# Kernel optimization log

Hardware: AMD Instinct MI355X
Metric: run time of the kernel (lower is better)

The kernel has to match this reference:

```python
import jax, jax.numpy as jnp
import numpy as np

N, T, V = 64, 512, 25
L = 2 * V
M = N * T * V          # total graph nodes after flattening
E = 2_000_000          # number of directed edges
DIM_NODE, HIDDEN = 2, 20
BN_EPS = 1e-5


def setup_inputs() -> dict:
    key = jax.random.key(0)
    ks = jax.random.split(key, 8)
    x = jax.random.normal(ks[0], (N, T, L), dtype=jnp.float32)
    edge_index = jax.random.randint(ks[1], (2, E), 0, M, dtype=jnp.int64)
    # GCNConv(2 -> 20): weight + bias (PyG applies lin before propagate, bias after)
    W1 = jax.random.normal(ks[2], (DIM_NODE, HIDDEN), dtype=jnp.float32) * (1.0 / np.sqrt(DIM_NODE))
    b1 = jnp.zeros((HIDDEN,), dtype=jnp.float32)
    # BatchNorm1d(20) affine params
    gamma = jnp.ones((HIDDEN,), dtype=jnp.float32)
    beta = jnp.zeros((HIDDEN,), dtype=jnp.float32)
    # GCNConv(20 -> 2)
    W2 = jax.random.normal(ks[3], (HIDDEN, DIM_NODE), dtype=jnp.float32) * (1.0 / np.sqrt(HIDDEN))
    b2 = jnp.zeros((DIM_NODE,), dtype=jnp.float32)
    return {"x": x, "edge_index": edge_index, "W1": W1, "b1": b1,
            "gamma": gamma, "beta": beta, "W2": W2, "b2": b2}


def _gcn_conv(h, row, col, norm, W, b, num_nodes):
    # PyG GCNConv: linear transform, normalized gather-scatter aggregation, bias.
    h = h @ W                                            # [M, d_out]
    msg = h[row] * norm[:, None]                         # gather + scale  [E+M, d_out]
    out = jax.ops.segment_sum(msg, col, num_segments=num_nodes)
    return out + b


def reference(x, edge_index, W1, b1, gamma, beta, W2, b2):
    n, t, l = x.shape
    v = l // 2
    m = n * t * v
    xf = x.reshape(m, 2)

    # gcn_norm with add_self_loops=True, symmetric normalization
    self_loop = jnp.arange(m, dtype=edge_index.dtype)
    row = jnp.concatenate([edge_index[0], self_loop])
    col = jnp.concatenate([edge_index[1], self_loop])
    deg = jax.ops.segment_sum(jnp.ones(row.shape[0], dtype=x.dtype), col, num_segments=m)
    dinv = jnp.where(deg > 0, jax.lax.rsqrt(deg), 0.0)
    norm = dinv[row] * dinv[col]

    h = _gcn_conv(xf, row, col, norm, W1, b1, m)         # [M, 20]

    # BatchNorm1d in training mode: biased batch statistics over node dim
    mean = jnp.mean(h, axis=0)
    var = jnp.mean(jnp.square(h - mean), axis=0)
    h = (h - mean) * jax.lax.rsqrt(var + BN_EPS) * gamma + beta
    h = jax.nn.relu(h)

    out = _gcn_conv(h, row, col, norm, W2, b2, m)        # [M, 2]
    return out.reshape(n, t, l)
```

## Files before the change

kernel.cpp:

```cpp
#include <hip/hip_runtime.h>
#include <stdint.h>

#define MNODES (64*512*25)
#define NEDGES 2000000
#define HID 20
#define BN_EPSF 1e-5f

#define NB 800
#define BSHIFT 10
#define BNODES 1024
#define CAP 3072
#define RB 1024
#define EPT 16
#define CHUNK (RB*EPT)
#define SB 512

typedef unsigned long long ull;

#define QSCALE 2048.0f
#define INV_Q  (1.0f/2048.0f)
#define FBIAS 65536

__device__ inline unsigned int pack_src(float x, float y){
    int ix = __float2int_rn(fminf(fmaxf(x, -15.9f), 15.9f) * QSCALE);
    int iy = __float2int_rn(fminf(fmaxf(y, -15.9f), 15.9f) * QSCALE);
    return ((unsigned int)(unsigned short)(short)ix) |
           (((unsigned int)(unsigned short)(short)iy) << 16);
}
__device__ inline ull msg_to_add(unsigned int m){
    int sx = (int)(short)(m & 0xffffu);
    int sy = (int)(short)(m >> 16);
    return ((ull)(unsigned int)(sx + FBIAS) << 38) | (1ull << 26)
         | (ull)(unsigned int)(sy + FBIAS);
}
__device__ inline void unpack_acc(ull a, int& ix, int& iy, int& cnt){
    cnt = (int)((a >> 26) & 0xFFFu);
    iy  = (int)(a & 0x3FFFFFFu) - cnt * FBIAS;
    ix  = (int)(a >> 38)        - cnt * FBIAS;
}


__global__ __launch_bounds__(RB) void k_reorder(const void* ei,
                                                unsigned int* binned,
                                                unsigned int* counts){
    __shared__ unsigned int lhist[NB];
    __shared__ unsigned int lbase[NB];
    __shared__ unsigned int sflag;
    int tid = threadIdx.x;
    if (tid == 0) sflag = 0;
    for (int i = tid; i < NB; i += RB) lhist[i] = 0;
    __syncthreads();
    if (tid < 128){
        unsigned int a = ((const unsigned int*)ei)[2*tid + 1];
        if (a) atomicOr(&sflag, 1u);
    }
    __syncthreads();
    bool is32 = (sflag != 0);

    unsigned int ent[EPT];
    int bkt[EPT];
    bool ok[EPT];
    #pragma unroll
    for (int k = 0; k < EPT; ++k){
        int e = blockIdx.x*CHUNK + k*RB + tid;
        ok[k] = (e < NEDGES);
        if (ok[k]){
            unsigned int r, c;
            if (is32){
                const int* p = (const int*)ei;
                r = (unsigned int)p[e]; c = (unsigned int)p[NEDGES + e];
            } else {
                const long long* p = (const long long*)ei;
                r = (unsigned int)p[e]; c = (unsigned int)p[NEDGES + e];
            }
            bkt[k] = (int)(c >> BSHIFT);
            ent[k] = r | ((c & (BNODES-1)) << 20);
            atomicAdd(&lhist[bkt[k]], 1u);
        }
    }
    __syncthreads();
    for (int i = tid; i < NB; i += RB){
        lbase[i] = (unsigned int)(i*CAP) + atomicAdd(&counts[i], lhist[i]);
        lhist[i] = 0;
    }
    __syncthreads();
    #pragma unroll
    for (int k = 0; k < EPT; ++k){
        if (ok[k]){
            int b = bkt[k];
            unsigned int pos = lbase[b] + atomicAdd(&lhist[b], 1u);
            if (pos < (unsigned int)((b+1)*CAP)) binned[pos] = ent[k];
        }
    }
}


template<bool FINAL>
__global__ __launch_bounds__(SB) void k_scatter_bin(const unsigned int* __restrict__ binned,
                                                    const unsigned int* __restrict__ counts,
                                                    const unsigned int* __restrict__ srcq,
                                                    float* outbuf,
                                                    unsigned short* deg16,
                                                    const float* __restrict__ b2,
                                                    float* stats){
    __shared__ ull accs[BNODES];
    __shared__ float ss[8];
    int b = blockIdx.x, tid = threadIdx.x;
    int base = b*BNODES;
    if (!FINAL && tid < 8) ss[tid] = 0.0f;
    #pragma unroll
    for (int n = tid; n < BNODES; n += SB)
        accs[n] = msg_to_add(srcq[base + n]);
    __syncthreads();

    unsigned int start = (unsigned int)(b*CAP);
    unsigned int cnt_b = counts[b];
    unsigned int end   = start + (cnt_b < CAP ? cnt_b : CAP);
    unsigned int i = start + tid;
    for (; i + 3u*SB < end; i += 4u*SB){
        unsigned int m0 = binned[i];
        unsigned int m1 = binned[i +   SB];
        unsigned int m2 = binned[i + 2u*SB];
        unsigned int m3 = binned[i + 3u*SB];
        unsigned int s0 = srcq[m0 & 0xfffffu];
        unsigned int s1 = srcq[m1 & 0xfffffu];
        unsigned int s2v = srcq[m2 & 0xfffffu];
        unsigned int s3 = srcq[m3 & 0xfffffu];
        atomicAdd(&accs[m0 >> 20], msg_to_add(s0));
        atomicAdd(&accs[m1 >> 20], msg_to_add(s1));
        atomicAdd(&accs[m2 >> 20], msg_to_add(s2v));
        atomicAdd(&accs[m3 >> 20], msg_to_add(s3));
    }
    for (; i < end; i += SB){
        unsigned int m = binned[i];
        atomicAdd(&accs[m >> 20], msg_to_add(srcq[m & 0xfffffu]));
    }
    __syncthreads();

    float su=0.f, sv=0.f, suu=0.f, suv=0.f, svv=0.f;
    #pragma unroll
    for (int n = tid; n < BNODES; n += SB){
        int ix, iy, dg;
        unpack_acc(accs[n], ix, iy, dg);
        float d = rsqrtf((float)dg);
        float u = (float)ix * INV_Q * d;
        float v = (float)iy * INV_Q * d;
        if (FINAL){
            float2 o; o.x = u + b2[0]; o.y = v + b2[1];
            ((float2*)outbuf)[base + n] = o;
        } else {
            deg16[base + n] = (unsigned short)dg;
            float2 o; o.x = u; o.y = v;
            ((float2*)outbuf)[base + n] = o;
            su += u; sv += v; suu += u*u; suv += u*v; svv += v*v;
        }
    }
    if (!FINAL){
        #pragma unroll
        for (int off=32; off; off>>=1){
            su  += __shfl_down(su,  off, 64);
            sv  += __shfl_down(sv,  off, 64);
            suu += __shfl_down(suu, off, 64);
            suv += __shfl_down(suv, off, 64);
            svv += __shfl_down(svv, off, 64);
        }
        if ((tid & 63) == 0){
            atomicAdd(&ss[0], su);  atomicAdd(&ss[1], sv);
            atomicAdd(&ss[2], suu); atomicAdd(&ss[3], suv);
            atomicAdd(&ss[4], svv);
        }
        __syncthreads();
        if (tid < 5) atomicAdd(&stats[tid], ss[tid]);
    }
}

__global__ __launch_bounds__(SB) void k_prepq(const unsigned int* __restrict__ binned,
                                              const unsigned int* __restrict__ counts,
                                              const float* __restrict__ xf,
                                              unsigned int* xnq){
    __shared__ unsigned int cnt[BNODES];
    int b = blockIdx.x, tid = threadIdx.x;
    #pragma unroll
    for (int n = tid; n < BNODES; n += SB) cnt[n] = 0;
    __syncthreads();
    unsigned int start = (unsigned int)(b*CAP);
    unsigned int cnt_b = counts[b];
    unsigned int end   = start + (cnt_b < CAP ? cnt_b : CAP);
    for (unsigned int i = start + tid; i < end; i += SB)
        atomicAdd(&cnt[binned[i] >> 20], 1u);
    __syncthreads();
    int base = b*BNODES;
    #pragma unroll
    for (int n = tid; n < BNODES; n += SB){
        float d = rsqrtf((float)(cnt[n] + 1u));
        float2 xv = ((const float2*)xf)[base + n];
        xnq[base + n] = pack_src(xv.x*d, xv.y*d);
    }
}

__global__ void k_project(const float* __restrict__ s2,
                          const unsigned short* __restrict__ deg16,
                          const float* __restrict__ W1, const float* __restrict__ b1,
                          const float* __restrict__ stats,
                          const float* __restrict__ gamma, const float* __restrict__ beta,
                          const float* __restrict__ W2,
                          unsigned int* pq){
    __shared__ float sc[2*HID];
    int tid = threadIdx.x;
    if (tid < HID){
        const float invM = 1.0f / (float)MNODES;
        float Su  = stats[0]*invM, Sv  = stats[1]*invM;
        float Suu = stats[2]*invM, Suv = stats[3]*invM, Svv = stats[4]*invM;
        float a = W1[tid], bb = W1[HID+tid], c = b1[tid];
        float mean = a*Su + bb*Sv + c;
        float ex2  = a*a*Suu + 2.f*a*bb*Suv + bb*bb*Svv
                   + 2.f*a*c*Su + 2.f*bb*c*Sv + c*c;
        float var  = ex2 - mean*mean;
        float inv  = rsqrtf(var + BN_EPSF);
        float scale = gamma[tid]*inv;
        sc[tid]     = scale;
        sc[HID+tid] = beta[tid] - mean*scale;
    }
    __syncthreads();
    int i = blockIdx.x*blockDim.x + tid;
    if (i >= MNODES) return;
    float2 s = ((const float2*)s2)[i];
    float d = rsqrtf((float)deg16[i]);
    float a0 = 0.0f, a1 = 0.0f;
    #pragma unroll
    for (int j=0;j<HID;++j){
        float h = s.x*W1[j] + s.y*W1[HID+j] + b1[j];
        float a = fmaxf(h*sc[j] + sc[HID+j], 0.0f);
        a0 += a*W2[2*j];
        a1 += a*W2[2*j+1];
    }
    pq[i] = pack_src(a0*d, a1*d);
}


extern "C" void kernel_launch(void* const* d_in, const int* in_sizes, int n_in,
                              void* d_out, int out_size, void* d_ws, size_t ws_size,
                              hipStream_t stream){
    const float* xf    = (const float*)d_in[0];
    const void*  ei    = d_in[1];
    const float* W1    = (const float*)d_in[2];
    const float* b1    = (const float*)d_in[3];
    const float* gamma = (const float*)d_in[4];
    const float* beta  = (const float*)d_in[5];
    const float* W2    = (const float*)d_in[6];
    const float* b2    = (const float*)d_in[7];
    float* out = (float*)d_out;

    char* ws = (char*)d_ws;
    size_t o = 0;
    auto carve = [&](size_t bytes)->char*{
        char* r = ws + o;
        o = (o + bytes + 255) & ~(size_t)255;
        return r;
    };
    unsigned int*   counts = (unsigned int*)  carve((size_t)NB*4);
    float*          stats  = (float*)         carve(8*4);
    unsigned int*   binned = (unsigned int*)  carve((size_t)NB*CAP*4);
    unsigned short* deg16  = (unsigned short*)carve((size_t)MNODES*2);
    unsigned int*   xnq    = (unsigned int*)  carve((size_t)MNODES*4);
    float*          s2     = (float*)         carve((size_t)MNODES*8);
    unsigned int*   pq     = (unsigned int*)  carve((size_t)MNODES*4);
    (void)ws_size; (void)in_sizes; (void)n_in; (void)out_size;

    const int gR = (NEDGES + CHUNK - 1) / CHUNK;
    const int gN = (MNODES + 255) / 256;

    hipMemsetAsync(counts, 0, (size_t)((char*)stats - (char*)counts) + 8*4, stream);
    hipLaunchKernelGGL(k_reorder, dim3(gR),  dim3(RB),  0, stream, ei, binned, counts);
    hipLaunchKernelGGL(k_prepq,   dim3(NB),  dim3(SB),  0, stream, binned, counts, xf, xnq);
    hipLaunchKernelGGL((k_scatter_bin<false>), dim3(NB), dim3(SB), 0, stream,
                       binned, counts, xnq, s2, deg16, b2, stats);
    hipLaunchKernelGGL(k_project, dim3(gN),  dim3(256), 0, stream,
                       s2, deg16, W1, b1, stats, gamma, beta, W2, pq);
    hipLaunchKernelGGL((k_scatter_bin<true>),  dim3(NB), dim3(SB), 0, stream,
                       binned, counts, pq, out, deg16, b2, stats);
}
```

Baseline: 83.52 us.

## Fuse post-reorder stages into one cooperative persistent kernel with grid syncs

Replaces the four launches that follow the reorder (prepq, first scatter, project, final scatter) with a single cooperative kernel of 512 blocks of 256 threads, separated by grid-wide syncs. If the cooperative launch fails it falls back to the separate kernels. Buckets become 800 nodes each, 1024 of them, using a multiply-shift divide-by-800, with block size cut to 256. The goal is to remove launch gaps and tail effects between stages. The cost is grid-sync overhead and possibly lower occupancy from the persistent grid size.

New measurement: 271.2 us. 3.25x slower.

```diff
diff --git a/kernel.cpp b/kernel.cpp
--- a/kernel.cpp
+++ b/kernel.cpp
@@ -1,25 +1,32 @@
 #include <hip/hip_runtime.h>
+#include <hip/hip_cooperative_groups.h>
 #include <stdint.h>
+
+namespace cg = cooperative_groups;
 
 #define MNODES (64*512*25)
 #define NEDGES 2000000
 #define HID 20
 #define BN_EPSF 1e-5f
 
-#define NB 800
-#define BSHIFT 10
-#define BNODES 1024
-#define CAP 3072
+#define NB 1024
+#define BNODES 800
+#define CAP 2432
 #define RB 1024
 #define EPT 16
 #define CHUNK (RB*EPT)
-#define SB 512
+#define GRID 512
+#define BLK 256
 
 typedef unsigned long long ull;
 
 #define QSCALE 2048.0f
 #define INV_Q  (1.0f/2048.0f)
 #define FBIAS 65536
+
+__device__ inline unsigned int div800(unsigned int c){
+    return (unsigned int)(((ull)c * 42949673ull) >> 35);
+}
 
 __device__ inline unsigned int pack_src(float x, float y){
     int ix = __float2int_rn(fminf(fmaxf(x, -15.9f), 15.9f) * QSCALE);
@@ -38,7 +45,6 @@
     iy  = (int)(a & 0x3FFFFFFu) - cnt * FBIAS;
     ix  = (int)(a >> 38)        - cnt * FBIAS;
 }
-
 
 __global__ __launch_bounds__(RB) void k_reorder(const void* ei,
                                                 unsigned int* binned,
@@ -73,9 +79,10 @@
                 const long long* p = (const long long*)ei;
                 r = (unsigned int)p[e]; c = (unsigned int)p[NEDGES + e];
             }
-            bkt[k] = (int)(c >> BSHIFT);
-            ent[k] = r | ((c & (BNODES-1)) << 20);
-            atomicAdd(&lhist[bkt[k]], 1u);
+            unsigned int q = div800(c);
+            bkt[k] = (int)q;
+            ent[k] = r | ((c - q*BNODES) << 20);
+            atomicAdd(&lhist[q], 1u);
         }
     }
     __syncthreads();
@@ -95,33 +102,51 @@
 }
 
 
+__device__ inline void prepq_bucket(int b, const unsigned int* __restrict__ binned,
+                                    const unsigned int* __restrict__ counts,
+                                    const float* __restrict__ xf,
+                                    unsigned int* xnq, ull* smem, int tid){
+    unsigned int* cnt = (unsigned int*)smem;
+    for (int n = tid; n < BNODES; n += BLK) cnt[n] = 0;
+    __syncthreads();
+    unsigned int start = (unsigned int)(b*CAP);
+    unsigned int cb = counts[b];
+    unsigned int end = start + (cb < CAP ? cb : CAP);
+    for (unsigned int i = start + tid; i < end; i += BLK)
+        atomicAdd(&cnt[binned[i] >> 20], 1u);
+    __syncthreads();
+    int base = b*BNODES;
+    for (int n = tid; n < BNODES; n += BLK){
+        float d = rsqrtf((float)(cnt[n] + 1u));
+        float2 xv = ((const float2*)xf)[base + n];
+        xnq[base + n] = pack_src(xv.x*d, xv.y*d);
+    }
+    __syncthreads();
+}
+
 template<bool FINAL>
-__global__ __launch_bounds__(SB) void k_scatter_bin(const unsigned int* __restrict__ binned,
-                                                    const unsigned int* __restrict__ counts,
-                                                    const unsigned int* __restrict__ srcq,
-                                                    float* outbuf,
-                                                    unsigned short* deg16,
-                                                    const float* __restrict__ b2,
-                                                    float* stats){
-    __shared__ ull accs[BNODES];
-    __shared__ float ss[8];
-    int b = blockIdx.x, tid = threadIdx.x;
+__device__ inline void scatter_bucket(int b, const unsigned int* __restrict__ binned,
+                                      const unsigned int* __restrict__ counts,
+                                      const unsigned int* __restrict__ srcq,
+                                      float* outbuf, unsigned short* deg16,
+                                      const float* __restrict__ b2, float* stats,
+                                      ull* accs, int tid){
+    float* ss = (float*)(accs + BNODES);
     int base = b*BNODES;
     if (!FINAL && tid < 8) ss[tid] = 0.0f;
-    #pragma unroll
-    for (int n = tid; n < BNODES; n += SB)
+    for (int n = tid; n < BNODES; n += BLK)
         accs[n] = msg_to_add(srcq[base + n]);
     __syncthreads();
 
     unsigned int start = (unsigned int)(b*CAP);
-    unsigned int cnt_b = counts[b];
-    unsigned int end   = start + (cnt_b < CAP ? cnt_b : CAP);
+    unsigned int cb = counts[b];
+    unsigned int end = start + (cb < CAP ? cb : CAP);
     unsigned int i = start + tid;
-    for (; i + 3u*SB < end; i += 4u*SB){
+    for (; i + 3u*BLK < end; i += 4u*BLK){
         unsigned int m0 = binned[i];
-        unsigned int m1 = binned[i +   SB];
-        unsigned int m2 = binned[i + 2u*SB];
-        unsigned int m3 = binned[i + 3u*SB];
+        unsigned int m1 = binned[i +   BLK];
+        unsigned int m2 = binned[i + 2u*BLK];
+        unsigned int m3 = binned[i + 3u*BLK];
         unsigned int s0 = srcq[m0 & 0xfffffu];
         unsigned int s1 = srcq[m1 & 0xfffffu];
         unsigned int s2v = srcq[m2 & 0xfffffu];
@@ -131,22 +156,23 @@
         atomicAdd(&accs[m2 >> 20], msg_to_add(s2v));
         atomicAdd(&accs[m3 >> 20], msg_to_add(s3));
     }
-    for (; i < end; i += SB){
+    for (; i < end; i += BLK){
         unsigned int m = binned[i];
         atomicAdd(&accs[m >> 20], msg_to_add(srcq[m & 0xfffffu]));
     }
     __syncthreads();
 
     float su=0.f, sv=0.f, suu=0.f, suv=0.f, svv=0.f;
-    #pragma unroll
-    for (int n = tid; n < BNODES; n += SB){
+    float bx = 0.f, by = 0.f;
+    if (FINAL){ bx = b2[0]; by = b2[1]; }
+    for (int n = tid; n < BNODES; n += BLK){
         int ix, iy, dg;
         unpack_acc(accs[n], ix, iy, dg);
         float d = rsqrtf((float)dg);
         float u = (float)ix * INV_Q * d;
         float v = (float)iy * INV_Q * d;
         if (FINAL){
-            float2 o; o.x = u + b2[0]; o.y = v + b2[1];
+            float2 o; o.x = u + bx; o.y = v + by;
             ((float2*)outbuf)[base + n] = o;
         } else {
             deg16[base + n] = (unsigned short)dg;
@@ -172,41 +198,13 @@
         __syncthreads();
         if (tid < 5) atomicAdd(&stats[tid], ss[tid]);
     }
-}
-
-__global__ __launch_bounds__(SB) void k_prepq(const unsigned int* __restrict__ binned,
-                                              const unsigned int* __restrict__ counts,
-                                              const float* __restrict__ xf,
-                                              unsigned int* xnq){
-    __shared__ unsigned int cnt[BNODES];
-    int b = blockIdx.x, tid = threadIdx.x;
-    #pragma unroll
-    for (int n = tid; n < BNODES; n += SB) cnt[n] = 0;
-    __syncthreads();
-    unsigned int start = (unsigned int)(b*CAP);
-    unsigned int cnt_b = counts[b];
-    unsigned int end   = start + (cnt_b < CAP ? cnt_b : CAP);
-    for (unsigned int i = start + tid; i < end; i += SB)
-        atomicAdd(&cnt[binned[i] >> 20], 1u);
-    __syncthreads();
-    int base = b*BNODES;
-    #pragma unroll
-    for (int n = tid; n < BNODES; n += SB){
-        float d = rsqrtf((float)(cnt[n] + 1u));
-        float2 xv = ((const float2*)xf)[base + n];
-        xnq[base + n] = pack_src(xv.x*d, xv.y*d);
-    }
-}
-
-__global__ void k_project(const float* __restrict__ s2,
-                          const unsigned short* __restrict__ deg16,
-                          const float* __restrict__ W1, const float* __restrict__ b1,
-                          const float* __restrict__ stats,
-                          const float* __restrict__ gamma, const float* __restrict__ beta,
-                          const float* __restrict__ W2,
-                          unsigned int* pq){
-    __shared__ float sc[2*HID];
-    int tid = threadIdx.x;
+    __syncthreads();
+}
+
+__device__ inline void bn_coeffs(const float* __restrict__ stats,
+                                 const float* __restrict__ W1, const float* __restrict__ b1,
+                                 const float* __restrict__ gamma, const float* __restrict__ beta,
+                                 float* sc, int tid){
     if (tid < HID){
         const float invM = 1.0f / (float)MNODES;
         float Su  = stats[0]*invM, Sv  = stats[1]*invM;
@@ -221,9 +219,13 @@
         sc[tid]     = scale;
         sc[HID+tid] = beta[tid] - mean*scale;
     }
-    __syncthreads();
-    int i = blockIdx.x*blockDim.x + tid;
-    if (i >= MNODES) return;
+}
+
+__device__ inline void project_node(int i, const float* __restrict__ s2,
+                                    const unsigned short* __restrict__ deg16,
+                                    const float* __restrict__ W1, const float* __restrict__ b1,
+                                    const float* __restrict__ W2, const float* sc,
+                                    unsigned int* pq){
     float2 s = ((const float2*)s2)[i];
     float d = rsqrtf((float)deg16[i]);
     float a0 = 0.0f, a1 = 0.0f;
@@ -235,6 +237,84 @@
         a1 += a*W2[2*j+1];
     }
     pq[i] = pack_src(a0*d, a1*d);
+}
+
+
+__global__ __launch_bounds__(BLK) void k_prepq(const unsigned int* __restrict__ binned,
+                                               const unsigned int* __restrict__ counts,
+                                               const float* __restrict__ xf,
+                                               unsigned int* xnq){
+    __shared__ ull smem[BNODES + 8];
+    prepq_bucket((int)blockIdx.x, binned, counts, xf, xnq, smem, threadIdx.x);
+}
+
+template<bool FINAL>
+__global__ __launch_bounds__(BLK) void k_scat(const unsigned int* __restrict__ binned,
+                                              const unsigned int* __restrict__ counts,
+                                              const unsigned int* __restrict__ srcq,
+                                              float* outbuf, unsigned short* deg16,
+                                              const float* __restrict__ b2, float* stats){
+    __shared__ ull smem[BNODES + 8];
+    scatter_bucket<FINAL>((int)blockIdx.x, binned, counts, srcq, outbuf, deg16,
+                          b2, stats, smem, threadIdx.x);
+}
+
+__global__ void k_project(const float* __restrict__ s2,
+                          const unsigned short* __restrict__ deg16,
+                          const float* __restrict__ W1, const float* __restrict__ b1,
+                          const float* __restrict__ stats,
+                          const float* __restrict__ gamma, const float* __restrict__ beta,
+                          const float* __restrict__ W2,
+                          unsigned int* pq){
+    __shared__ float sc[2*HID];
+    bn_coeffs(stats, W1, b1, gamma, beta, sc, threadIdx.x);
+    __syncthreads();
+    int i = blockIdx.x*blockDim.x + threadIdx.x;
+    if (i < MNODES) project_node(i, s2, deg16, W1, b1, W2, sc, pq);
+}
+
+
+struct MP {
+    const float* xf;
+    const float* W1; const float* b1;
+    const float* gamma; const float* beta;
+    const float* W2; const float* b2;
+    float* out;
+    const unsigned int* binned;
+    const unsigned int* counts;
+    unsigned short* deg16;
+    unsigned int* xnq;
+    float* s2;
+    unsigned int* pq;
+    float* stats;
+};
+
+__global__ __launch_bounds__(BLK, 2) void k_mega(MP P){
+    __shared__ ull smem[BNODES + 8];
+    cg::grid_group g = cg::this_grid();
+    const int tid = threadIdx.x;
+
+    for (int b = (int)blockIdx.x; b < NB; b += GRID)
+        prepq_bucket(b, P.binned, P.counts, P.xf, P.xnq, smem, tid);
+    g.sync();
+
+    for (int b = (int)blockIdx.x; b < NB; b += GRID)
+        scatter_bucket<false>(b, P.binned, P.counts, P.xnq, P.s2, P.deg16,
+                              P.b2, P.stats, smem, tid);
+    g.sync();
+
+    {
+        float* sc = (float*)smem;
+        bn_coeffs(P.stats, P.W1, P.b1, P.gamma, P.beta, sc, tid);
+        __syncthreads();
+        for (int i = (int)blockIdx.x*BLK + tid; i < MNODES; i += GRID*BLK)
+            project_node(i, P.s2, P.deg16, P.W1, P.b1, P.W2, sc, P.pq);
+    }
+    g.sync();
+
+    for (int b = (int)blockIdx.x; b < NB; b += GRID)
+        scatter_bucket<true>(b, P.binned, P.counts, P.pq, P.out, P.deg16,
+                             P.b2, P.stats, smem, tid);
 }
 
 
@@ -267,16 +347,29 @@
     unsigned int*   pq     = (unsigned int*)  carve((size_t)MNODES*4);
     (void)ws_size; (void)in_sizes; (void)n_in; (void)out_size;
 
+    hipMemsetAsync(counts, 0, (size_t)((char*)stats - (char*)counts) + 8*4, stream);
+
     const int gR = (NEDGES + CHUNK - 1) / CHUNK;
-    const int gN = (MNODES + 255) / 256;
-
-    hipMemsetAsync(counts, 0, (size_t)((char*)stats - (char*)counts) + 8*4, stream);
-    hipLaunchKernelGGL(k_reorder, dim3(gR),  dim3(RB),  0, stream, ei, binned, counts);
-    hipLaunchKernelGGL(k_prepq,   dim3(NB),  dim3(SB),  0, stream, binned, counts, xf, xnq);
-    hipLaunchKernelGGL((k_scatter_bin<false>), dim3(NB), dim3(SB), 0, stream,
-                       binned, counts, xnq, s2, deg16, b2, stats);
-    hipLaunchKernelGGL(k_project, dim3(gN),  dim3(256), 0, stream,
-                       s2, deg16, W1, b1, stats, gamma, beta, W2, pq);
-    hipLaunchKernelGGL((k_scatter_bin<true>),  dim3(NB), dim3(SB), 0, stream,
-                       binned, counts, pq, out, deg16, b2, stats);
-}
+    hipLaunchKernelGGL(k_reorder, dim3(gR), dim3(RB), 0, stream, ei, binned, counts);
+
+    MP mp;
+    mp.xf = xf; mp.W1 = W1; mp.b1 = b1; mp.gamma = gamma; mp.beta = beta;
+    mp.W2 = W2; mp.b2 = b2; mp.out = out;
+    mp.binned = binned; mp.counts = counts;
+    mp.deg16 = deg16; mp.xnq = xnq; mp.s2 = s2; mp.pq = pq; mp.stats = stats;
+    void* args[] = { &mp };
+    hipError_t cerr = hipLaunchCooperativeKernel((void*)k_mega, dim3(GRID), dim3(BLK),
+                                                 args, 0, stream);
+    if (cerr != hipSuccess){
+        (void)hipGetLastError();
+        const int gN = (MNODES + 255) / 256;
+        hipLaunchKernelGGL(k_prepq,        dim3(NB), dim3(BLK), 0, stream,
+                           binned, counts, xf, xnq);
+        hipLaunchKernelGGL((k_scat<false>), dim3(NB), dim3(BLK), 0, stream,
+                           binned, counts, xnq, s2, deg16, b2, stats);
+        hipLaunchKernelGGL(k_project,      dim3(gN), dim3(256), 0, stream,
+                           s2, deg16, W1, b1, stats, gamma, beta, W2, pq);
+        hipLaunchKernelGGL((k_scat<true>),  dim3(NB), dim3(BLK), 0, stream,
+                           binned, counts, pq, out, deg16, b2, stats);
+    }
+}
```
